# Kernel optimization log

Hardware: AMD Instinct MI355X
Metric: run time of the kernel (lower is better)

Reference implementation:

```python
import jax, jax.numpy as jnp
import numpy as np
from jax import lax

B, S, CIN, COUT, K = 32, 2048, 256, 256, 16


def setup_inputs() -> dict:
    key = jax.random.key(0)
    k1, k2, k3, k4 = jax.random.split(key, 4)
    x = jax.random.normal(k1, (B, S, CIN), dtype=jnp.float32)
    w_real = jax.random.normal(k2, (COUT, CIN, K), dtype=jnp.float32) * 0.1
    w_imag = jax.random.normal(k3, (COUT, CIN, K), dtype=jnp.float32) * 0.1
    phases = jax.random.normal(k4, (K,), dtype=jnp.float32) * 0.1
    return {"x": x, "w_real": w_real, "w_imag": w_imag, "phases": phases}


def reference(x, w_real, w_imag, phases):
    # out[b,t,o] = Re( sum_{k,i} x[b,t+k,i] * exp(1j*phases[k]) * (w_real + 1j*w_imag)[o,i,k] )
    # x is real, so this equals a real valid conv1d with effective kernel:
    #   w_eff[o,i,k] = cos(phases[k]) * w_real[o,i,k] - sin(phases[k]) * w_imag[o,i,k]
    w_eff = jnp.cos(phases)[None, None, :] * w_real - jnp.sin(phases)[None, None, :] * w_imag
    # conv expects NCH / OIH layouts
    y = lax.conv_general_dilated(
        jnp.transpose(x, (0, 2, 1)),  # [B, CIN, S]
        w_eff,                         # [COUT, CIN, K]
        window_strides=(1,),
        padding="VALID",
        dimension_numbers=("NCH", "OIH", "NCH"),
    )
    return jnp.transpose(y, (0, 2, 1))  # [B, S-K+1, COUT]
```

## Files before the change

kernel.cpp:

```cpp
#include <hip/hip_runtime.h>
#include <math.h>

#define B_    32
#define S_    2048
#define CIN_  256
#define COUT_ 256
#define K_    16
#define TOUT_ 2033
#define RTOT_ 4096

typedef __bf16 bf16x4 __attribute__((ext_vector_type(4)));
typedef __bf16 bf16x8 __attribute__((ext_vector_type(8)));
typedef float  f32x16 __attribute__((ext_vector_type(16)));

#define GLOBAL_AS __attribute__((address_space(1)))
#define LDS_AS    __attribute__((address_space(3)))

__device__ __forceinline__ void gload_lds16(const void* g, void* l) {
  __builtin_amdgcn_global_load_lds((const GLOBAL_AS void*)g, (LDS_AS void*)l, 16, 0, 0);
}

__global__ void __launch_bounds__(256) build_wt_kernel(const float* __restrict__ wr,
                                                       const float* __restrict__ wi,
                                                       const float* __restrict__ ph,
                                                       __bf16* __restrict__ wt) {
  int t = blockIdx.x * 256 + threadIdx.x;
  int o = t >> 8, i = t & 255;
  const float4* wr4 = (const float4*)(wr + (size_t)(o * CIN_ + i) * K_);
  const float4* wi4 = (const float4*)(wi + (size_t)(o * CIN_ + i) * K_);
  float re[16], im[16];
  #pragma unroll
  for (int v = 0; v < 4; v++) {
    float4 a = wr4[v];
    re[4*v+0]=a.x; re[4*v+1]=a.y; re[4*v+2]=a.z; re[4*v+3]=a.w;
    float4 b = wi4[v];
    im[4*v+0]=b.x; im[4*v+1]=b.y; im[4*v+2]=b.z; im[4*v+3]=b.w;
  }
  const int ob = o >> 5, s = (i >> 4) & 1, kh = (i >> 3) & 1;
  const int olow = o & 31, j = i & 7;
  const int ic = i >> 5;
  #pragma unroll
  for (int kk = 0; kk < K_; kk++) {
    float p = ph[kk];
    int c = kk * 8 + ic;
    int addr = (((c * 8 + ob) * 4 + s * 2 + kh) * 256) + olow * 8 + j;
    wt[addr] = (__bf16)(cosf(p)*re[kk] - sinf(p)*im[kk]);
  }
}

__global__ void __launch_bounds__(256) conv_mfma_kernel(const float* __restrict__ xg,
                                                        const __bf16* __restrict__ wt,
                                                        float* __restrict__ out) {
  __shared__ __align__(16) __bf16 As[4 * 145 * 8];
  __shared__ __align__(16) __bf16 Bs[4096];

  const int bx = blockIdx.x;
  const int nb = bx & 1;
  const int mb = (bx >> 1) & 15;
  const int b  = bx >> 5;

  const int tid  = threadIdx.x;
  const int w    = tid >> 6;
  const int lane = tid & 63;
  const int wm   = w >> 1, wn = w & 1;
  const int l31  = lane & 31, lhi = lane >> 5;

  const int t0 = mb * 128;
  const int o0 = nb * 128;

  const float*  xbase  = xg + (size_t)b * (S_ * CIN_);
  const __bf16* wtbase = wt + nb * 4096;

  const int sr = tid >> 3;
  const int sc = (tid & 7) * 4;
  const int sp = sc >> 3;
  const int sj = sc & 7;

  f32x16 acc[2][2];
  #pragma unroll
  for (int jm = 0; jm < 2; jm++)
    #pragma unroll
    for (int jn = 0; jn < 2; jn++)
      #pragma unroll
      for (int r = 0; r < 16; r++)
        acc[jm][jn][r] = 0.f;

  for (int ic = 0; ic < 8; ++ic) {
    const int i0 = ic * 32;

    __syncthreads();

    {
      const float* xcol = xbase + i0 + sc;
      #pragma unroll
      for (int p = 0; p < 4; p++) {
        int r = p * 32 + sr;
        int rg = t0 + r; rg = (rg < S_) ? rg : (S_ - 1);
        float4 v = *(const float4*)(xcol + (size_t)rg * CIN_);
        bf16x4 o4; o4[0]=(__bf16)v.x; o4[1]=(__bf16)v.y; o4[2]=(__bf16)v.z; o4[3]=(__bf16)v.w;
        *(bf16x4*)(As + (sp * 145 + r) * 8 + sj) = o4;
      }
      if (tid < 128) {
        int r = 128 + sr;
        int rg = t0 + r; rg = (rg < S_) ? rg : (S_ - 1);
        float4 v = *(const float4*)(xcol + (size_t)rg * CIN_);
        bf16x4 o4; o4[0]=(__bf16)v.x; o4[1]=(__bf16)v.y; o4[2]=(__bf16)v.z; o4[3]=(__bf16)v.w;
        *(bf16x4*)(As + (sp * 145 + r) * 8 + sj) = o4;
      }
    }

    for (int kk = 0; kk < K_; ++kk) {
      if (kk) __syncthreads();

      const __bf16* gb = wtbase + (size_t)(kk * 8 + ic) * 8192;
      #pragma unroll
      for (int p = 0; p < 2; p++) {
        int seg = w * 2 + p;
        gload_lds16(gb + seg * 512 + lane * 8, (void*)(Bs + seg * 512));
      }

      __syncthreads();

      bf16x8 af[2][2], bfr[2][2];
      #pragma unroll
      for (int jm = 0; jm < 2; jm++)
        #pragma unroll
        for (int s = 0; s < 2; s++) {
          int row = kk + wm * 64 + jm * 32 + l31;
          af[jm][s] = *(const bf16x8*)(As + ((s * 2 + lhi) * 145 + row) * 8);
        }
      #pragma unroll
      for (int jn = 0; jn < 2; jn++)
        #pragma unroll
        for (int s = 0; s < 2; s++) {
          int grp = (wn * 2 + jn) * 4 + s * 2 + lhi;
          bfr[jn][s] = *(const bf16x8*)(Bs + grp * 256 + l31 * 8);
        }

      #pragma unroll
      for (int s = 0; s < 2; s++)
        #pragma unroll
        for (int jm = 0; jm < 2; jm++)
          #pragma unroll
          for (int jn = 0; jn < 2; jn++)
            acc[jm][jn] = __builtin_amdgcn_mfma_f32_32x32x16_bf16(af[jm][s], bfr[jn][s], acc[jm][jn], 0, 0, 0);
    }
  }

  float* obase = out + (size_t)b * TOUT_ * COUT_;
  #pragma unroll
  for (int jm = 0; jm < 2; jm++) {
    #pragma unroll
    for (int reg = 0; reg < 16; reg++) {
      int rowcd = (reg & 3) + 8 * (reg >> 2) + 4 * lhi;
      int t = t0 + wm * 64 + jm * 32 + rowcd;
      if (t < TOUT_) {
        float* orow = obase + (size_t)t * COUT_ + o0 + wn * 64 + l31;
        #pragma unroll
        for (int jn = 0; jn < 2; jn++)
          orow[jn * 32] = acc[jm][jn][reg];
      }
    }
  }
}

extern "C" void kernel_launch(void* const* d_in, const int* in_sizes, int n_in,
                              void* d_out, int out_size, void* d_ws, size_t ws_size,
                              hipStream_t stream) {
  const float* x  = (const float*)d_in[0];
  const float* wr = (const float*)d_in[1];
  const float* wi = (const float*)d_in[2];
  const float* ph = (const float*)d_in[3];
  float* out = (float*)d_out;

  __bf16* wt = (__bf16*)d_ws;

  build_wt_kernel<<<dim3((COUT_ * CIN_) / 256), dim3(256), 0, stream>>>(wr, wi, ph, wt);
  conv_mfma_kernel<<<dim3(B_ * 16 * 2), dim3(256), 0, stream>>>(x, wt, out);
}
```

Measured before the change: 268.8 us.

## Stage full input tile in LDS once and read weights directly into registers

The whole 145-row by 256-channel bf16 input tile is loaded into LDS once up front, about 74KB. Weight fragments are read straight from global memory into registers instead of through an LDS buffer. All 128 (channel-chunk, tap) steps then run as one loop with register double-buffering and no barriers. This removes the 256 per-step __syncthreads and the repeated LDS staging of weights. The cost is higher LDS use, which limits occupancy to about two blocks per CU, and weight loads that depend on L2/global latency being hidden by the one-step prefetch.

After: 243.9 us. -9.3%, faster.

```diff
diff --git a/kernel.cpp b/kernel.cpp
--- a/kernel.cpp
+++ b/kernel.cpp
@@ -7,18 +7,10 @@
 #define COUT_ 256
 #define K_    16
 #define TOUT_ 2033
-#define RTOT_ 4096
 
 typedef __bf16 bf16x4 __attribute__((ext_vector_type(4)));
 typedef __bf16 bf16x8 __attribute__((ext_vector_type(8)));
 typedef float  f32x16 __attribute__((ext_vector_type(16)));
-
-#define GLOBAL_AS __attribute__((address_space(1)))
-#define LDS_AS    __attribute__((address_space(3)))
-
-__device__ __forceinline__ void gload_lds16(const void* g, void* l) {
-  __builtin_amdgcn_global_load_lds((const GLOBAL_AS void*)g, (LDS_AS void*)l, 16, 0, 0);
-}
 
 __global__ void __launch_bounds__(256) build_wt_kernel(const float* __restrict__ wr,
                                                        const float* __restrict__ wi,
@@ -48,11 +40,12 @@
   }
 }
 
+#define PR 145
+
 __global__ void __launch_bounds__(256) conv_mfma_kernel(const float* __restrict__ xg,
                                                         const __bf16* __restrict__ wt,
                                                         float* __restrict__ out) {
-  __shared__ __align__(16) __bf16 As[4 * 145 * 8];
-  __shared__ __align__(16) __bf16 Bs[4096];
+  __shared__ __align__(16) __bf16 As[32 * PR * 8];
 
   const int bx = blockIdx.x;
   const int nb = bx & 1;
@@ -68,13 +61,59 @@
   const int t0 = mb * 128;
   const int o0 = nb * 128;
 
-  const float*  xbase  = xg + (size_t)b * (S_ * CIN_);
-  const __bf16* wtbase = wt + nb * 4096;
+  const float* xbase = xg + (size_t)b * (S_ * CIN_);
 
-  const int sr = tid >> 3;
-  const int sc = (tid & 7) * 4;
-  const int sp = sc >> 3;
-  const int sj = sc & 7;
+  {
+    const int sr  = tid >> 3;
+    const int sc4 = (tid & 7) * 4;
+    const int spl = sc4 >> 3;
+    const int sj  = sc4 & 7;
+    for (int ic = 0; ic < 8; ++ic) {
+      const float* xcol = xbase + ic * 32 + sc4;
+      __bf16* dst = As + ((ic * 4 + spl) * PR) * 8 + sj;
+      #pragma unroll
+      for (int p = 0; p < 4; p++) {
+        int r = p * 32 + sr;
+        int rg = t0 + r; rg = (rg < S_) ? rg : (S_ - 1);
+        float4 v = *(const float4*)(xcol + (size_t)rg * CIN_);
+        bf16x4 o4; o4[0]=(__bf16)v.x; o4[1]=(__bf16)v.y; o4[2]=(__bf16)v.z; o4[3]=(__bf16)v.w;
+        *(bf16x4*)(dst + r * 8) = o4;
+      }
+      if (tid < 128) {
+        int r = 128 + sr;
+        int rg = t0 + r; rg = (rg < S_) ? rg : (S_ - 1);
+        float4 v = *(const float4*)(xcol + (size_t)rg * CIN_);
+        bf16x4 o4; o4[0]=(__bf16)v.x; o4[1]=(__bf16)v.y; o4[2]=(__bf16)v.z; o4[3]=(__bf16)v.w;
+        *(bf16x4*)(dst + r * 8) = o4;
+      }
+    }
+  }
+  __syncthreads();
+
+  const __bf16* bptr[2] = {
+    wt + (size_t)nb * 4096 + (wn * 2 + 0) * 1024 + lane * 8,
+    wt + (size_t)nb * 4096 + (wn * 2 + 1) * 1024 + lane * 8
+  };
+  const int arow = wm * 64 + l31;
+
+  auto load_a = [&](int g, bf16x8 (&af)[2][2]) {
+    int ic = g >> 4, kk = g & 15;
+    #pragma unroll
+    for (int jm = 0; jm < 2; jm++)
+      #pragma unroll
+      for (int s = 0; s < 2; s++) {
+        int plane = ic * 4 + s * 2 + lhi;
+        af[jm][s] = *(const bf16x8*)(As + (plane * PR + kk + arow + jm * 32) * 8);
+      }
+  };
+  auto load_b = [&](int g, bf16x8 (&bf)[2][2]) {
+    size_t co = (size_t)(((g & 15) << 3) + (g >> 4)) * 8192;
+    #pragma unroll
+    for (int jn = 0; jn < 2; jn++)
+      #pragma unroll
+      for (int s = 0; s < 2; s++)
+        bf[jn][s] = *(const bf16x8*)(bptr[jn] + co + s * 512);
+  };
 
   f32x16 acc[2][2];
   #pragma unroll
@@ -85,66 +124,24 @@
       for (int r = 0; r < 16; r++)
         acc[jm][jn][r] = 0.f;
 
-  for (int ic = 0; ic < 8; ++ic) {
-    const int i0 = ic * 32;
+  bf16x8 ab[2][2][2], bb[2][2][2];
+  load_a(0, ab[0]);
+  load_b(0, bb[0]);
 
-    __syncthreads();
-
-    {
-      const float* xcol = xbase + i0 + sc;
-      #pragma unroll
-      for (int p = 0; p < 4; p++) {
-        int r = p * 32 + sr;
-        int rg = t0 + r; rg = (rg < S_) ? rg : (S_ - 1);
-        float4 v = *(const float4*)(xcol + (size_t)rg * CIN_);
-        bf16x4 o4; o4[0]=(__bf16)v.x; o4[1]=(__bf16)v.y; o4[2]=(__bf16)v.z; o4[3]=(__bf16)v.w;
-        *(bf16x4*)(As + (sp * 145 + r) * 8 + sj) = o4;
-      }
-      if (tid < 128) {
-        int r = 128 + sr;
-        int rg = t0 + r; rg = (rg < S_) ? rg : (S_ - 1);
-        float4 v = *(const float4*)(xcol + (size_t)rg * CIN_);
-        bf16x4 o4; o4[0]=(__bf16)v.x; o4[1]=(__bf16)v.y; o4[2]=(__bf16)v.z; o4[3]=(__bf16)v.w;
-        *(bf16x4*)(As + (sp * 145 + r) * 8 + sj) = o4;
-      }
-    }
-
-    for (int kk = 0; kk < K_; ++kk) {
-      if (kk) __syncthreads();
-
-      const __bf16* gb = wtbase + (size_t)(kk * 8 + ic) * 8192;
-      #pragma unroll
-      for (int p = 0; p < 2; p++) {
-        int seg = w * 2 + p;
-        gload_lds16(gb + seg * 512 + lane * 8, (void*)(Bs + seg * 512));
-      }
-
-      __syncthreads();
-
-      bf16x8 af[2][2], bfr[2][2];
+  #pragma unroll 2
+  for (int g = 0; g < 128; ++g) {
+    const int cur = g & 1, nxt = cur ^ 1;
+    const int gn = (g < 127) ? g + 1 : 127;
+    load_a(gn, ab[nxt]);
+    load_b(gn, bb[nxt]);
+    #pragma unroll
+    for (int s = 0; s < 2; s++)
       #pragma unroll
       for (int jm = 0; jm < 2; jm++)
         #pragma unroll
-        for (int s = 0; s < 2; s++) {
-          int row = kk + wm * 64 + jm * 32 + l31;
-          af[jm][s] = *(const bf16x8*)(As + ((s * 2 + lhi) * 145 + row) * 8);
-        }
-      #pragma unroll
-      for (int jn = 0; jn < 2; jn++)
-        #pragma unroll
-        for (int s = 0; s < 2; s++) {
-          int grp = (wn * 2 + jn) * 4 + s * 2 + lhi;
-          bfr[jn][s] = *(const bf16x8*)(Bs + grp * 256 + l31 * 8);
-        }
-
-      #pragma unroll
-      for (int s = 0; s < 2; s++)
-        #pragma unroll
-        for (int jm = 0; jm < 2; jm++)
-          #pragma unroll
-          for (int jn = 0; jn < 2; jn++)
-            acc[jm][jn] = __builtin_amdgcn_mfma_f32_32x32x16_bf16(af[jm][s], bfr[jn][s], acc[jm][jn], 0, 0, 0);
-    }
+        for (int jn = 0; jn < 2; jn++)
+          acc[jm][jn] = __builtin_amdgcn_mfma_f32_32x32x16_bf16(
+              ab[cur][jm][s], bb[cur][jn][s], acc[jm][jn], 0, 0, 0);
   }
 
   float* obase = out + (size_t)b * TOUT_ * COUT_;
@@ -156,9 +153,8 @@
       int t = t0 + wm * 64 + jm * 32 + rowcd;
       if (t < TOUT_) {
         float* orow = obase + (size_t)t * COUT_ + o0 + wn * 64 + l31;
-        #pragma unroll
-        for (int jn = 0; jn < 2; jn++)
-          orow[jn * 32] = acc[jm][jn][reg];
+        orow[0]  = acc[jm][0][reg];
+        orow[32] = acc[jm][1][reg];
       }
     }
   }
```
